# Optimization experiments

Hardware: AMD Instinct MI355X
Metric: run time of the kernel (lower is better)

Reference implementation:

```python
import jax, jax.numpy as jnp
import numpy as np

N_NODES = 100000
NUM_LAYER = 3
REG_WEIGHT = 1e-4


def setup_inputs() -> dict:
    key = jax.random.key(0)
    ks = jax.random.split(key, 6)
    E = 1280000
    B = 4096
    D = 64
    # xavier-uniform-like scale for embedding table
    emb_weight = jax.random.normal(ks[0], (N_NODES, D), dtype=jnp.float32) * 0.01
    src = jax.random.randint(ks[1], (E,), 0, N_NODES, dtype=jnp.int32)
    dst = jax.random.randint(ks[2], (E,), 0, N_NODES, dtype=jnp.int32)
    users = jax.random.randint(ks[3], (B,), 0, N_NODES, dtype=jnp.int32)
    pos = jax.random.randint(ks[4], (B,), 0, N_NODES, dtype=jnp.int32)
    neg = jax.random.randint(ks[5], (B,), 0, N_NODES, dtype=jnp.int32)
    return {"emb_weight": emb_weight, "src": src, "dst": dst,
            "users": users, "pos": pos, "neg": neg}


def _edge_norm(src, dst):
    # DGL norm(): d = sum of edge mask (ones) per dst node; adj_e = d[src]^-0.5 * d[dst]^-0.5
    ones = jnp.ones(src.shape[0], dtype=jnp.float32)
    deg = jax.ops.segment_sum(ones, dst, num_segments=N_NODES)
    dinv = jnp.where(deg > 0, deg ** -0.5, 0.0)  # inf -> 0 handling
    return dinv[src] * dinv[dst]  # [E]


def _propagate(emb_weight, src, dst, adj):
    # LightGCN propagation: h_{l+1}[v] = sum_{(u->v)} adj_e * h_l[u]
    h = emb_weight
    layers = [h]
    for _ in range(NUM_LAYER):
        m = h[src] * adj[:, None]                    # [E, D] gather + edge weight
        h = jax.ops.segment_sum(m, dst, num_segments=N_NODES)  # [N, D] scatter-sum
        layers.append(h)
    return jnp.mean(jnp.stack(layers, axis=1), axis=1)  # mean over L+1 layers


def reference(emb_weight, src, dst, users, pos, neg):
    adj = _edge_norm(src, dst)
    all_emb = _propagate(emb_weight, src, dst, adj)

    u_e, p_e, n_e = all_emb[users], all_emb[pos], all_emb[neg]
    u0, p0, n0 = emb_weight[users], emb_weight[pos], emb_weight[neg]

    B = users.shape[0]
    reg_loss = 0.5 * (jnp.sum(u0 ** 2) + jnp.sum(p0 ** 2) + jnp.sum(n0 ** 2)) / B
    reg_loss = reg_loss * REG_WEIGHT

    pos_scores = jnp.sum(u_e * p_e, axis=1)
    neg_scores = jnp.sum(u_e * n_e, axis=1)
    loss_emb = jnp.mean(jax.nn.softplus(neg_scores - pos_scores))

    loss = loss_emb + reg_loss
    return loss, loss_emb, reg_loss
```

## Files before the change

### kernel.cpp

```cpp
#include <hip/hip_runtime.h>
#include <hip/hip_fp8.h>
#include <math.h>

#define N_NODES 100000
#define DIM 64
#define NUM_LAYER 3
#define BATCH 4096
#define REG_WEIGHT 1e-4f
#define NBUCKET 391
#define STAGE_CAP 4096
#define CURPAD 16
#define H_SCALE 256.0f
#define H_INV_SCALE (1.0f / 256.0f)

typedef float floatx2 __attribute__((ext_vector_type(2)));

__device__ unsigned char g_hf8[2][(size_t)N_NODES * DIM];
__device__ float g_sums[(size_t)3 * BATCH * DIM];
__device__ int   g_row_ptr[N_NODES + 1];
__device__ float g_dinv[N_NODES];
__device__ int   g_bcur[NBUCKET * CURPAD];
__device__ unsigned int g_stage[NBUCKET * STAGE_CAP];
__device__ int   g_csr[1280000];
__device__ int   g_shead[N_NODES];
__device__ int   g_snext[3 * BATCH];
__device__ float g_part_sp[BATCH];
__device__ float g_part_rg[BATCH];

__device__ inline void fma4_fp8(unsigned int d, float w,
                                float& a0, float& a1, float& a2, float& a3) {
    floatx2 lo = __builtin_amdgcn_cvt_pk_f32_fp8((int)d, false);
    floatx2 hi = __builtin_amdgcn_cvt_pk_f32_fp8((int)d, true);
    a0 = fmaf(w, lo.x, a0); a1 = fmaf(w, lo.y, a1);
    a2 = fmaf(w, hi.x, a2); a3 = fmaf(w, hi.y, a3);
}
__device__ inline unsigned int pack4_fp8(float a0, float a1, float a2, float a3) {
    int w = __builtin_amdgcn_cvt_pk_fp8_f32(a0, a1, 0, false);
    w     = __builtin_amdgcn_cvt_pk_fp8_f32(a2, a3, w, true);
    return (unsigned int)w;
}

#define EDGES_PER_THREAD 8
__global__ void __launch_bounds__(1024) stage_buckets(const int* __restrict__ src,
                                                      const int* __restrict__ dst, int E,
                                                      const int* __restrict__ users,
                                                      const int* __restrict__ pos,
                                                      const int* __restrict__ neg) {
    __shared__ int h[NBUCKET];
    __shared__ int cur[NBUCKET];
    int tid = threadIdx.x;
    int gt = blockIdx.x * 1024 + tid;
    if (gt < 3 * BATCH) {
        int which = gt / BATCH, s = gt - which * BATCH;
        const int* idx = (which == 0) ? users : ((which == 1) ? pos : neg);
        g_snext[gt] = atomicExch(&g_shead[idx[s]], gt + 1);
    }
    int base = blockIdx.x * (1024 * EDGES_PER_THREAD);
    for (int i = tid; i < NBUCKET; i += 1024) h[i] = 0;
    __syncthreads();
    int myd[EDGES_PER_THREAD], mys[EDGES_PER_THREAD];
    #pragma unroll
    for (int k = 0; k < EDGES_PER_THREAD; ++k) {
        int e = base + k * 1024 + tid;
        if (e < E) {
            myd[k] = dst[e]; mys[k] = src[e];
            atomicAdd(&h[myd[k] >> 8], 1);
        } else myd[k] = -1;
    }
    __syncthreads();
    for (int i = tid; i < NBUCKET; i += 1024) {
        int c = h[i];
        cur[i] = c ? (atomicAdd(&g_bcur[i * CURPAD], c) + i * STAGE_CAP) : 0;
    }
    __syncthreads();
    #pragma unroll
    for (int k = 0; k < EDGES_PER_THREAD; ++k) {
        if (myd[k] >= 0) {
            int p = atomicAdd(&cur[myd[k] >> 8], 1);
            g_stage[p] = (unsigned int)((mys[k] << 8) | (myd[k] & 255));
        }
    }
}

__global__ void __launch_bounds__(512) finalize_place(const float* __restrict__ emb) {
    __shared__ int cs[512];
    __shared__ int lh[256], sc[256], cur[256];
    __shared__ float ldv[256];
    int b = blockIdx.x, t = threadIdx.x;
    int c = (t < NBUCKET) ? g_bcur[t * CURPAD] : 0;
    cs[t] = c;
    __syncthreads();
    for (int off = 1; off < 512; off <<= 1) {
        int x = (t >= off) ? cs[t - off] : 0;
        __syncthreads();
        cs[t] += x;
        __syncthreads();
    }
    int mybase = (b > 0) ? cs[b - 1] : 0;
    int cnt    = cs[b] - mybase;
    if (b == 0 && t == 0) g_row_ptr[N_NODES] = cs[NBUCKET - 1];
    int sbeg = b * STAGE_CAP;
    if (t < 256) lh[t] = 0;
    __syncthreads();
    for (int k = t; k < cnt; k += 512)
        atomicAdd(&lh[g_stage[sbeg + k] & 255], 1);
    __syncthreads();
    int v = 0;
    if (t < 256) { v = lh[t]; sc[t] = v; }
    __syncthreads();
    for (int off = 1; off < 256; off <<= 1) {
        int x = (t >= off && t < 256) ? sc[t - off] : 0;
        __syncthreads();
        if (t < 256) sc[t] += x;
        __syncthreads();
    }
    if (t < 256) {
        int start = mybase + sc[t] - v;
        cur[t] = start;
        float dv = (v > 0) ? rsqrtf((float)v) : 0.0f;
        ldv[t] = dv;
        int node = (b << 8) + t;
        if (node < N_NODES) {
            g_row_ptr[node] = start;
            g_dinv[node]    = dv;
        }
    }
    __syncthreads();
    for (int k = t; k < cnt; k += 512) {
        unsigned int e = g_stage[sbeg + k];
        int pos = atomicAdd(&cur[e & 255], 1);
        g_csr[pos] = (int)(e >> 8);
    }
    {
        int nbase = b << 8;
        int rows = N_NODES - nbase; if (rows > 256) rows = 256;
        unsigned int* hw = (unsigned int*)g_hf8[0];
        for (int idx = t; idx < rows * 16; idx += 512) {
            int row = idx >> 4, li = idx & 15;
            const float4 ev = *(const float4*)(emb + (size_t)(nbase + row) * DIM + li * 4);
            float s = ldv[row] * H_SCALE;
            hw[(size_t)(nbase + row) * 16 + li] =
                pack4_fp8(ev.x * s, ev.y * s, ev.z * s, ev.w * s);
        }
    }
}

__global__ void pull_layer_fp8(const unsigned char* __restrict__ h,
                               unsigned char* __restrict__ hn, int mode) {
    int gid0 = blockIdx.x * blockDim.x + threadIdx.x;
    if (mode == 1 && gid0 < NBUCKET) g_bcur[gid0 * CURPAD] = 0;
    int wid  = gid0 >> 6;
    int lane = threadIdx.x & 63;
    int g  = lane >> 4;
    int li = lane & 15;
    int n = wid * 4 + g;
    if (n >= N_NODES) return;
    int beg = g_row_ptr[n], end = g_row_ptr[n + 1];
    float dinvN = g_dinv[n];
    float a0 = 0.f, a1 = 0.f, a2 = 0.f, a3 = 0.f;
    for (int k = beg; k < end; k += 4) {
        int k1 = min(k + 1, end - 1);
        int k2 = min(k + 2, end - 1);
        int k3 = min(k + 3, end - 1);
        int s0 = g_csr[k];
        int s1 = g_csr[k1];
        int s2 = g_csr[k2];
        int s3 = g_csr[k3];
        unsigned int d0 = *(const unsigned int*)(h + (size_t)s0 * DIM + li * 4);
        unsigned int d1 = *(const unsigned int*)(h + (size_t)s1 * DIM + li * 4);
        unsigned int d2 = *(const unsigned int*)(h + (size_t)s2 * DIM + li * 4);
        unsigned int d3 = *(const unsigned int*)(h + (size_t)s3 * DIM + li * 4);
        float w1 = (k + 1 < end) ? 1.0f : 0.0f;
        float w2 = (k + 2 < end) ? 1.0f : 0.0f;
        float w3 = (k + 3 < end) ? 1.0f : 0.0f;
        fma4_fp8(d0, 1.0f, a0, a1, a2, a3);
        fma4_fp8(d1, w1, a0, a1, a2, a3);
        fma4_fp8(d2, w2, a0, a1, a2, a3);
        fma4_fp8(d3, w3, a0, a1, a2, a3);
    }
    float dd = dinvN * dinvN;
    *(unsigned int*)(hn + (size_t)n * DIM + li * 4) =
        pack4_fp8(a0 * dd, a1 * dd, a2 * dd, a3 * dd);
    if (mode) {
        float gw = dinvN * H_INV_SCALE;
        int sidx = g_shead[n];
        while (sidx > 0) {
            int sr = sidx - 1;
            float* sp = &g_sums[(size_t)sr * DIM + li * 4];
            if (mode == 1) {
                sp[0] = a0 * gw; sp[1] = a1 * gw;
                sp[2] = a2 * gw; sp[3] = a3 * gw;
            } else {
                sp[0] += a0 * gw; sp[1] += a1 * gw;
                sp[2] += a2 * gw; sp[3] += a3 * gw;
            }
            sidx = g_snext[sr];
        }
        if (mode == 2 && li == 0) g_shead[n] = 0;
    }
}

__global__ void pull_sampled(const unsigned char* __restrict__ h,
                             const int* __restrict__ users, const int* __restrict__ pos,
                             const int* __restrict__ neg) {
    int gid0 = blockIdx.x * blockDim.x + threadIdx.x;
    int wid  = gid0 >> 6;
    int lane = threadIdx.x & 63;
    int g  = lane >> 4;
    int li = lane & 15;
    int s = wid * 4 + g;
    if (s >= 3 * BATCH) return;
    int which = s >> 12;
    int i     = s & (BATCH - 1);
    const int* idx = (which == 0) ? users : ((which == 1) ? pos : neg);
    int node = idx[i];
    int beg = g_row_ptr[node], end = g_row_ptr[node + 1];
    float dinvN = g_dinv[node];
    float a0 = 0.f, a1 = 0.f, a2 = 0.f, a3 = 0.f;
    for (int k = beg; k < end; k += 4) {
        int k1 = min(k + 1, end - 1);
        int k2 = min(k + 2, end - 1);
        int k3 = min(k + 3, end - 1);
        int s0 = g_csr[k];
        int s1 = g_csr[k1];
        int s2 = g_csr[k2];
        int s3 = g_csr[k3];
        unsigned int d0 = *(const unsigned int*)(h + (size_t)s0 * DIM + li * 4);
        unsigned int d1 = *(const unsigned int*)(h + (size_t)s1 * DIM + li * 4);
        unsigned int d2 = *(const unsigned int*)(h + (size_t)s2 * DIM + li * 4);
        unsigned int d3 = *(const unsigned int*)(h + (size_t)s3 * DIM + li * 4);
        float w1 = (k + 1 < end) ? 1.0f : 0.0f;
        float w2 = (k + 2 < end) ? 1.0f : 0.0f;
        float w3 = (k + 3 < end) ? 1.0f : 0.0f;
        fma4_fp8(d0, 1.0f, a0, a1, a2, a3);
        fma4_fp8(d1, w1, a0, a1, a2, a3);
        fma4_fp8(d2, w2, a0, a1, a2, a3);
        fma4_fp8(d3, w3, a0, a1, a2, a3);
    }
    float gw = dinvN * H_INV_SCALE;
    float* sp = &g_sums[(size_t)s * DIM + li * 4];
    sp[0] += a0 * gw;
    sp[1] += a1 * gw;
    sp[2] += a2 * gw;
    sp[3] += a3 * gw;
}

__global__ void score_reduce(const float* __restrict__ emb,
                             const int* __restrict__ users, const int* __restrict__ pos,
                             const int* __restrict__ neg) {
    int wid  = (blockIdx.x * blockDim.x + threadIdx.x) >> 6;
    int lane = threadIdx.x & 63;
    if (wid >= BATCH) return;
    float u0 = emb[(size_t)users[wid] * DIM + lane];
    float p0 = emb[(size_t)pos[wid]   * DIM + lane];
    float n0 = emb[(size_t)neg[wid]   * DIM + lane];
    float u = 0.25f * (g_sums[(size_t)wid * DIM + lane] + u0);
    float p = 0.25f * (g_sums[(size_t)(BATCH + wid) * DIM + lane] + p0);
    float n = 0.25f * (g_sums[(size_t)(2 * BATCH + wid) * DIM + lane] + n0);
    float ps = u * p;
    float ns = u * n;
    float rg = u0 * u0 + p0 * p0 + n0 * n0;
    #pragma unroll
    for (int off = 32; off > 0; off >>= 1) {
        ps += __shfl_down(ps, off);
        ns += __shfl_down(ns, off);
        rg += __shfl_down(rg, off);
    }
    if (lane == 0) {
        float x  = ns - ps;
        float sp = fmaxf(x, 0.0f) + log1pf(expf(-fabsf(x)));
        g_part_sp[wid] = sp;
        g_part_rg[wid] = rg;
    }
}

__global__ void final_reduce(float* __restrict__ out) {
    __shared__ float s_sp[256], s_rg[256];
    int t = threadIdx.x;
    float sp = 0.0f, rg = 0.0f;
    for (int i = t; i < BATCH; i += 256) { sp += g_part_sp[i]; rg += g_part_rg[i]; }
    s_sp[t] = sp; s_rg[t] = rg;
    __syncthreads();
    for (int off = 128; off > 0; off >>= 1) {
        if (t < off) { s_sp[t] += s_sp[t + off]; s_rg[t] += s_rg[t + off]; }
        __syncthreads();
    }
    if (t == 0) {
        float loss_emb = s_sp[0] / (float)BATCH;
        float reg      = 0.5f * s_rg[0] / (float)BATCH * REG_WEIGHT;
        out[0] = loss_emb + reg;
        out[1] = loss_emb;
        out[2] = reg;
    }
}

extern "C" void kernel_launch(void* const* d_in, const int* in_sizes, int n_in,
                              void* d_out, int out_size, void* d_ws, size_t ws_size,
                              hipStream_t stream) {
    const float* emb   = (const float*)d_in[0];
    const int*   src   = (const int*)d_in[1];
    const int*   dst   = (const int*)d_in[2];
    const int*   users = (const int*)d_in[3];
    const int*   pos   = (const int*)d_in[4];
    const int*   neg   = (const int*)d_in[5];
    const int E = in_sizes[1];
    float* out = (float*)d_out;

    unsigned char* hf_a;  hipGetSymbolAddress((void**)&hf_a, HIP_SYMBOL(g_hf8));
    unsigned char* hf_b = hf_a + (size_t)N_NODES * DIM;

    const int STAGE_BLOCKS = (E + 1024 * EDGES_PER_THREAD - 1) / (1024 * EDGES_PER_THREAD);
    stage_buckets<<<STAGE_BLOCKS, 1024, 0, stream>>>(src, dst, E, users, pos, neg);
    finalize_place<<<NBUCKET, 512, 0, stream>>>(emb);

    const int NQUAD = (N_NODES + 3) / 4;
    const int PULL_BLOCKS = (NQUAD * 64 + 255) / 256;

    pull_layer_fp8<<<PULL_BLOCKS, 256, 0, stream>>>(hf_a, hf_b, 1);

    pull_layer_fp8<<<PULL_BLOCKS, 256, 0, stream>>>(hf_b, hf_a, 2);

    const int SAMP_BLOCKS = ((3 * BATCH + 3) / 4 * 64 + 255) / 256;
    pull_sampled<<<SAMP_BLOCKS, 256, 0, stream>>>(hf_a, users, pos, neg);

    score_reduce<<<(BATCH * 64 + 255) / 256, 256, 0, stream>>>(emb, users, pos, neg);
    final_reduce<<<1, 256, 0, stream>>>(out);
}
```

Measured before the change: 182.1 us.

## Use finer 64-node buckets for CSR staging and finalize with more smaller blocks

Shrinks the destination bucket width from 256 nodes to 64, giving 1563 buckets and 1563 finalize blocks of 256 threads instead of 391 blocks of 512. Each finalize block now computes its base offset by summing preceding bucket counts rather than doing a full block-wide prefix scan. The aim is better GPU occupancy and shorter per-block serial work in the CSR placement step. In exchange, stage_buckets has more shared-memory histogram bins and global bucket atomics. The later blocks also re-read up to 1562 counts each, and per-bucket capacity drops to 1280, which leaves less headroom above the mean of about 820 edges per bucket.

```diff
diff --git a/kernel.cpp b/kernel.cpp
--- a/kernel.cpp
+++ b/kernel.cpp
@@ -7,8 +7,10 @@
 #define NUM_LAYER 3
 #define BATCH 4096
 #define REG_WEIGHT 1e-4f
-#define NBUCKET 391
-#define STAGE_CAP 4096
+#define NBUCKET 1563
+#define BSHIFT 6
+#define BMASK 63
+#define STAGE_CAP 1280
 #define CURPAD 16
 #define H_SCALE 256.0f
 #define H_INV_SCALE (1.0f / 256.0f)
@@ -64,7 +66,7 @@
         int e = base + k * 1024 + tid;
         if (e < E) {
             myd[k] = dst[e]; mys[k] = src[e];
-            atomicAdd(&h[myd[k] >> 8], 1);
+            atomicAdd(&h[myd[k] >> BSHIFT], 1);
         } else myd[k] = -1;
     }
     __syncthreads();
@@ -76,66 +78,64 @@
     #pragma unroll
     for (int k = 0; k < EDGES_PER_THREAD; ++k) {
         if (myd[k] >= 0) {
-            int p = atomicAdd(&cur[myd[k] >> 8], 1);
-            g_stage[p] = (unsigned int)((mys[k] << 8) | (myd[k] & 255));
+            int p = atomicAdd(&cur[myd[k] >> BSHIFT], 1);
+            g_stage[p] = (unsigned int)((mys[k] << BSHIFT) | (myd[k] & BMASK));
         }
     }
 }
 
-__global__ void __launch_bounds__(512) finalize_place(const float* __restrict__ emb) {
-    __shared__ int cs[512];
-    __shared__ int lh[256], sc[256], cur[256];
-    __shared__ float ldv[256];
+__global__ void __launch_bounds__(256) finalize_place(const float* __restrict__ emb) {
+    __shared__ int red[256];
+    __shared__ int lh[64], sc[64], cur[64];
+    __shared__ float ldv[64];
     int b = blockIdx.x, t = threadIdx.x;
-    int c = (t < NBUCKET) ? g_bcur[t * CURPAD] : 0;
-    cs[t] = c;
-    __syncthreads();
-    for (int off = 1; off < 512; off <<= 1) {
-        int x = (t >= off) ? cs[t - off] : 0;
+    int sum = 0;
+    for (int i = t; i < b; i += 256) sum += g_bcur[i * CURPAD];
+    red[t] = sum;
+    __syncthreads();
+    for (int off = 128; off > 0; off >>= 1) {
+        if (t < off) red[t] += red[t + off];
         __syncthreads();
-        cs[t] += x;
+    }
+    int bbase = red[0];
+    int cnt   = g_bcur[b * CURPAD];
+    if (b == NBUCKET - 1 && t == 0) g_row_ptr[N_NODES] = bbase + cnt;
+    int sbeg = b * STAGE_CAP;
+    if (t < 64) lh[t] = 0;
+    __syncthreads();
+    for (int k = t; k < cnt; k += 256)
+        atomicAdd(&lh[g_stage[sbeg + k] & BMASK], 1);
+    __syncthreads();
+    int v = 0;
+    if (t < 64) { v = lh[t]; sc[t] = v; }
+    __syncthreads();
+    for (int off = 1; off < 64; off <<= 1) {
+        int x = (t >= off && t < 64) ? sc[t - off] : 0;
         __syncthreads();
-    }
-    int mybase = (b > 0) ? cs[b - 1] : 0;
-    int cnt    = cs[b] - mybase;
-    if (b == 0 && t == 0) g_row_ptr[N_NODES] = cs[NBUCKET - 1];
-    int sbeg = b * STAGE_CAP;
-    if (t < 256) lh[t] = 0;
-    __syncthreads();
-    for (int k = t; k < cnt; k += 512)
-        atomicAdd(&lh[g_stage[sbeg + k] & 255], 1);
-    __syncthreads();
-    int v = 0;
-    if (t < 256) { v = lh[t]; sc[t] = v; }
-    __syncthreads();
-    for (int off = 1; off < 256; off <<= 1) {
-        int x = (t >= off && t < 256) ? sc[t - off] : 0;
+        if (t < 64) sc[t] += x;
         __syncthreads();
-        if (t < 256) sc[t] += x;
-        __syncthreads();
-    }
-    if (t < 256) {
-        int start = mybase + sc[t] - v;
+    }
+    int nbase = b << BSHIFT;
+    int rows = N_NODES - nbase; if (rows > 64) rows = 64;
+    if (t < 64) {
+        int start = bbase + sc[t] - v;
         cur[t] = start;
         float dv = (v > 0) ? rsqrtf((float)v) : 0.0f;
         ldv[t] = dv;
-        int node = (b << 8) + t;
-        if (node < N_NODES) {
-            g_row_ptr[node] = start;
-            g_dinv[node]    = dv;
+        if (t < rows) {
+            g_row_ptr[nbase + t] = start;
+            g_dinv[nbase + t]    = dv;
         }
     }
     __syncthreads();
-    for (int k = t; k < cnt; k += 512) {
+    for (int k = t; k < cnt; k += 256) {
         unsigned int e = g_stage[sbeg + k];
-        int pos = atomicAdd(&cur[e & 255], 1);
-        g_csr[pos] = (int)(e >> 8);
+        int pos = atomicAdd(&cur[e & BMASK], 1);
+        g_csr[pos] = (int)(e >> BSHIFT);
     }
     {
-        int nbase = b << 8;
-        int rows = N_NODES - nbase; if (rows > 256) rows = 256;
         unsigned int* hw = (unsigned int*)g_hf8[0];
-        for (int idx = t; idx < rows * 16; idx += 512) {
+        for (int idx = t; idx < rows * 16; idx += 256) {
             int row = idx >> 4, li = idx & 15;
             const float4 ev = *(const float4*)(emb + (size_t)(nbase + row) * DIM + li * 4);
             float s = ldv[row] * H_SCALE;
@@ -311,7 +311,7 @@
 
     const int STAGE_BLOCKS = (E + 1024 * EDGES_PER_THREAD - 1) / (1024 * EDGES_PER_THREAD);
     stage_buckets<<<STAGE_BLOCKS, 1024, 0, stream>>>(src, dst, E, users, pos, neg);
-    finalize_place<<<NBUCKET, 512, 0, stream>>>(emb);
+    finalize_place<<<NBUCKET, 256, 0, stream>>>(emb);
 
     const int NQUAD = (N_NODES + 3) / 4;
     const int PULL_BLOCKS = (NQUAD * 64 + 255) / 256;
```

After: 185.2 us. No clear change (+1.7%).
